# Kernel tuning notes

Measured on AMD Instinct MI355X. Metric: run time of the kernel, lower is better.

The kernel has to match this reference:

```python
import jax, jax.numpy as jnp
import numpy as np

B, T, E, H, C = 64, 256, 1024, 1024, 32000


def setup_inputs() -> dict:
    key = jax.random.key(0)
    ks = jax.random.split(key, 8)
    s = 0.02
    return {
        "X": jax.random.randint(ks[0], (B, T), 0, C),
        "emb": jax.random.normal(ks[1], (C, E), jnp.float32) * s,
        "Wi1": jax.random.normal(ks[2], (4, H, E), jnp.float32) * s,
        "Wh1": jax.random.normal(ks[3], (4, H, H), jnp.float32) * s,
        "bi1": jnp.ones((4, H), jnp.float32),
        "bh1": jnp.ones((4, H), jnp.float32),
        "Wi2": jax.random.normal(ks[4], (4, H, E), jnp.float32) * s,
        "Wh2": jax.random.normal(ks[5], (4, H, H), jnp.float32) * s,
        "bi2": jnp.ones((4, H), jnp.float32),
        "bh2": jnp.ones((4, H), jnp.float32),
        "W": jax.random.normal(ks[6], (C, H), jnp.float32) * s,
        "b": jnp.ones((C,), jnp.float32),
    }


def _lstm_last_o(x_tbe, Wi, Wh, bi, bh):
    """Run LSTM over time; return the LAST output gate o_T, shape [B, H].

    x_tbe: [T, B, E]; Wi: [4, H, E]; Wh: [4, H, H]; bi, bh: [4, H]
    Gate order g = 0:i, 1:f, 2:g(cell cand), 3:o. Original module adds BOTH
    biases (b_i_* + b_h_*) every step.
    """
    Tn, Bn = x_tbe.shape[0], x_tbe.shape[1]
    Hn = Wh.shape[1]
    # Precompute input projections for all timesteps: [T, B, 4, H]
    xp = jnp.einsum('tbe,ghe->tbgh', x_tbe, Wi) + bi + bh

    def step(carry, xp_t):
        h, c, _ = carry
        g = xp_t + jnp.einsum('bh,gkh->bgk', h, Wh)  # [B, 4, H]
        i_t = jax.nn.sigmoid(g[:, 0])
        f_t = jax.nn.sigmoid(g[:, 1])
        g_t = jnp.tanh(g[:, 2])
        o_t = jax.nn.sigmoid(g[:, 3])
        c_new = f_t * c + i_t * g_t
        h_new = o_t * jnp.tanh(c_new)
        return (h_new, c_new, o_t), None

    z = jnp.zeros((Bn, Hn), x_tbe.dtype)
    (h_f, c_f, o_f), _ = jax.lax.scan(step, (z, z, z), xp)
    return o_f


def reference(X, emb, Wi1, Wh1, bi1, bh1, Wi2, Wh2, bi2, bh2, W, b):
    x = emb[X]                     # [B, T, E]
    xt = jnp.transpose(x, (1, 0, 2))  # [T, B, E]
    o1 = _lstm_last_o(xt, Wi1, Wh1, bi1, bh1)           # forward direction
    o2 = _lstm_last_o(xt[::-1], Wi2, Wh2, bi2, bh2)     # reversed direction
    return (o1 + o2) @ W.T + b      # [B, n_class]
```

## Files before the change

### kernel.cpp

```cpp
#include <hip/hip_runtime.h>
#include <hip/hip_bf16.h>
#include <stdint.h>

typedef __attribute__((ext_vector_type(4))) float    f32x4;
typedef __attribute__((ext_vector_type(8))) short    bf16x8;
typedef __attribute__((ext_vector_type(4))) uint32_t u32x4;
typedef unsigned short u16;

#define T_   256
#define B_   64
#define E_   1024
#define H_   1024
#define CLS  32000
#define NWG  256

#define OFF_XBF   0ull
#define OFF_CNT   OFF_XBF
#define OFF_WIALL 33554432ull
#define OFF_XP    50331648ull
#define OFF_WHP   318767104ull
#define OFF_BSUM  335544320ull
#define OFF_OBUF  336101376ull
#define OFF_OSUM  336625664ull
#define OFF_HROT  336756736ull
#define HROT_END  404127744ull

__device__ __forceinline__ u16 f2bf(float f) {
    union { float f; uint32_t i; } v; v.f = f;
    uint32_t r = v.i + 0x7fffu + ((v.i >> 16) & 1u);
    return (u16)(r >> 16);
}
__device__ __forceinline__ float bf2f(u16 u) {
    union { uint32_t i; float f; } v; v.i = ((uint32_t)u) << 16; return v.f;
}
__device__ __forceinline__ float sigm(float x)   { return 1.f / (1.f + __expf(-x)); }
__device__ __forceinline__ float tanh_f(float x) { return 1.f - 2.f / (__expf(2.f * x) + 1.f); }

__device__ __forceinline__ void ldg4_cc(unsigned& d, const unsigned* p) {
    asm volatile("global_load_dword %0, %1, off sc0 sc1"
                 : "=v"(d) : "v"(p) : "memory");
}
__device__ __forceinline__ void stg16_cc(u16* p, bf16x8 v) {
    asm volatile("global_store_dwordx4 %0, %1, off sc0 sc1"
                 :: "v"(p), "v"(v) : "memory");
}
__device__ __forceinline__ void stg4_cc(unsigned* p, unsigned v) {
    asm volatile("global_store_dword %0, %1, off sc0 sc1"
                 :: "v"(p), "v"(v) : "memory");
}
__device__ __forceinline__ void wait_vm0() {
    asm volatile("s_waitcnt vmcnt(0)" ::: "memory");
}


__global__ void k_gather(const int* __restrict__ X, const float* __restrict__ emb,
                         u16* __restrict__ xbf) {
    const int m = blockIdx.x;
    const int t = m >> 6, b = m & 63;
    const int tok = X[b * T_ + t];
    const float* src = emb + (size_t)tok * E_;
    u16* dst = xbf + (size_t)m * E_;
    const int e = threadIdx.x * 4;
    float4 v = *(const float4*)(src + e);
    ushort4 o; o.x = f2bf(v.x); o.y = f2bf(v.y); o.z = f2bf(v.z); o.w = f2bf(v.w);
    *(ushort4*)(dst + e) = o;
}

__global__ void k_cvt(const float* __restrict__ src, u16* __restrict__ dst) {
    const int i = (blockIdx.x * 256 + threadIdx.x) * 4;
    float4 v = *(const float4*)(src + i);
    ushort4 o; o.x = f2bf(v.x); o.y = f2bf(v.y); o.z = f2bf(v.z); o.w = f2bf(v.w);
    *(ushort4*)(dst + i) = o;
}

__global__ void k_packwh(const float* __restrict__ Wh1, const float* __restrict__ Wh2,
                         u16* __restrict__ whp) {
    const int gi  = blockIdx.x * 256 + threadIdx.x;
    const int wg  = gi >> 12;
    const int lin = gi & 4095;
    const int kc  = lin & 127;
    const int col = lin >> 7;
    const int dir = wg >> 7, hblk = wg & 127;
    const int g = col >> 3, hh = col & 7;
    const float* src = (dir ? Wh2 : Wh1) + (size_t)(g * H_ + hblk * 8 + hh) * H_ + kc * 8;
    float4 v0 = *(const float4*)(src);
    float4 v1 = *(const float4*)(src + 4);
    const uint32_t boff = (uint32_t)(((kc * 32 + col) * 16) ^ ((kc & 3) << 4));
    u16* dst = whp + (size_t)wg * 32768 + boff / 2;
    ushort4 o0, o1;
    o0.x = f2bf(v0.x); o0.y = f2bf(v0.y); o0.z = f2bf(v0.z); o0.w = f2bf(v0.w);
    o1.x = f2bf(v1.x); o1.y = f2bf(v1.y); o1.z = f2bf(v1.z); o1.w = f2bf(v1.w);
    *(ushort4*)dst = o0;
    *(ushort4*)(dst + 4) = o1;
}

__global__ void k_bias(const float* __restrict__ bi1, const float* __restrict__ bh1,
                       const float* __restrict__ bi2, const float* __restrict__ bh2,
                       float* __restrict__ bsum) {
    const int i = blockIdx.x * 256 + threadIdx.x;
    bsum[i] = (i < 4096) ? (bi1[i] + bh1[i]) : (bi2[i - 4096] + bh2[i - 4096]);
}


#define GLDS16(gp, lp) __builtin_amdgcn_global_load_lds( \
    (const __attribute__((address_space(1))) uint32_t*)(gp), \
    (__attribute__((address_space(3))) uint32_t*)(lp), 16, 0, 0)

__global__ __launch_bounds__(256) void k_gemm_xp(const u16* __restrict__ A,
                                                 const u16* __restrict__ Bw,
                                                 u16* __restrict__ Cp) {
    __shared__ __align__(16) u16 As[128 * 32];
    __shared__ __align__(16) u16 Bs[128 * 32];
    const int bid = blockIdx.x;
    const int bn = bid & 63, bm = bid >> 6;
    const int tid = threadIdx.x;
    const int wid = tid >> 6, lane = tid & 63;
    const int wm = wid & 1, wn = wid >> 1;
    const int col16 = lane & 15, kslot = lane >> 4;
    const char* Abase = (const char*)A + (size_t)bm * 128 * 2048;
    const char* Bbase = (const char*)Bw + (size_t)bn * 128 * 2048;
    const int rowoff = (lane >> 2) * 2048 + (lane & 3) * 16;
    f32x4 acc[4][4] = {};
    for (int kt = 0; kt < 32; ++kt) {
        const int ko = kt * 64;
#pragma unroll
        for (int q = 0; q < 2; ++q) {
            const int ci = q * 4 + wid;
            GLDS16(Abase + (size_t)ci * 16 * 2048 + rowoff + ko, (char*)As + ci * 1024);
            GLDS16(Bbase + (size_t)ci * 16 * 2048 + rowoff + ko, (char*)Bs + ci * 1024);
        }
        __syncthreads();
        bf16x8 af[4], bfr[4];
#pragma unroll
        for (int mi = 0; mi < 4; ++mi)
            af[mi] = *(const bf16x8*)(As + (wm * 64 + mi * 16 + col16) * 32 + kslot * 8);
#pragma unroll
        for (int ni = 0; ni < 4; ++ni)
            bfr[ni] = *(const bf16x8*)(Bs + (wn * 64 + ni * 16 + col16) * 32 + kslot * 8);
#pragma unroll
        for (int mi = 0; mi < 4; ++mi)
#pragma unroll
            for (int ni = 0; ni < 4; ++ni)
                acc[mi][ni] = __builtin_amdgcn_mfma_f32_16x16x32_bf16(af[mi], bfr[ni], acc[mi][ni], 0, 0, 0);
        __syncthreads();
    }
#pragma unroll
    for (int mi = 0; mi < 4; ++mi)
#pragma unroll
        for (int ni = 0; ni < 4; ++ni)
#pragma unroll
            for (int q = 0; q < 4; ++q) {
                const int r  = bm * 128 + wm * 64 + mi * 16 + kslot * 4 + q;
                const int cn = bn * 128 + wn * 64 + ni * 16 + col16;
                const int dircol = cn >> 12, c = cn & 4095;
                const int g = c >> 10, hidx = c & 1023;
                const int wgc = dircol * 128 + (hidx >> 3), fhc = hidx & 7;
                Cp[((size_t)r * 256 + wgc) * 32 + fhc * 4 + g] = f2bf(acc[mi][ni][q]);
            }
}

__global__ __launch_bounds__(512, 1) void k_lstm(
    const u16* __restrict__ xp, const u16* __restrict__ whp,
    const float* __restrict__ bsum, u16* hrot,
    float* __restrict__ obuf, unsigned* cnt) {
    __shared__ __align__(16) u16 wlds[32768];
    __shared__ float glds[2][64][35];
    __shared__ __align__(16) u16 hxch[64][8];
    const int wg = blockIdx.x;
    const int dir = wg >> 7, hblk = wg & 127;
    const int tid = threadIdx.x;
    const int wid = tid >> 6, lane = tid & 63;
    const int mtile = wid & 3, khalf = wid >> 2;
    const int col16 = lane & 15, kslot = lane >> 4;
    {
        const u32x4* s = (const u32x4*)(whp + (size_t)wg * 32768);
        u32x4* d = (u32x4*)wlds;
#pragma unroll
        for (int i = 0; i < 8; ++i) d[tid + i * 512] = s[tid + i * 512];
    }
    const int fb = tid >> 3, fh = tid & 7;
    const int hidx = hblk * 8 + fh;
    const int arow = mtile * 16 + col16;
    float bsF[4];
#pragma unroll
    for (int g = 0; g < 4; ++g) bsF[g] = bsum[dir * 4096 + g * 1024 + hidx];
    const unsigned* pollp = cnt + (size_t)(dir * 128 + khalf * 64 + lane) * 32;
    unsigned* flag_own = cnt + (size_t)(dir * 128 + hblk) * 32;
    float cc = 0.f;
    ushort4 xv;
    xv = *(const ushort4*)(xp + ((size_t)((dir ? (T_ - 1) : 0) * 64 + fb) * 256 + wg) * 32 + fh * 4);
    __syncthreads();
    for (int s = 0; s < T_; ++s) {
        if (s > 0) {
            const unsigned target = (unsigned)s;
            for (;;) {
                unsigned f;
                ldg4_cc(f, pollp);
                wait_vm0();
                if (__all(f >= target)) break;
                __builtin_amdgcn_s_sleep(1);
            }
        }
        __builtin_amdgcn_sched_barrier(0);
        const u16* hbase = hrot + (size_t)(s * 2 + dir) * 131072
                         + (size_t)(khalf * 64) * 512 + arow * 8;
        bf16x8 hf[16];
#pragma unroll
        for (int kk = 0; kk < 16; ++kk)
            hf[kk] = *(const bf16x8*)(hbase + (size_t)(kk * 4 + kslot) * 512);
        f32x4 acc0 = {0.f, 0.f, 0.f, 0.f}, acc1 = {0.f, 0.f, 0.f, 0.f};
#pragma unroll
        for (int kk = 0; kk < 16; ++kk) {
            const int kc = khalf * 64 + kk * 4 + kslot;
            const uint32_t base = (uint32_t)(kc * 512);
            const uint32_t sw = (uint32_t)((kc & 3) << 4);
            bf16x8 b0 = *(const bf16x8*)((const char*)wlds + ((base + (uint32_t)(col16 * 16)) ^ sw));
            bf16x8 b1 = *(const bf16x8*)((const char*)wlds + ((base + (uint32_t)(256 + col16 * 16)) ^ sw));
            acc0 = __builtin_amdgcn_mfma_f32_16x16x32_bf16(hf[kk], b0, acc0, 0, 0, 0);
            acc1 = __builtin_amdgcn_mfma_f32_16x16x32_bf16(hf[kk], b1, acc1, 0, 0, 0);
        }
#pragma unroll
        for (int q = 0; q < 4; ++q) {
            glds[khalf][mtile * 16 + kslot * 4 + q][col16]      = acc0[q];
            glds[khalf][mtile * 16 + kslot * 4 + q][16 + col16] = acc1[q];
        }
        __syncthreads();
        const float gi = glds[0][fb][fh]      + glds[1][fb][fh]      + bsF[0] + bf2f(xv.x);
        const float gf = glds[0][fb][8 + fh]  + glds[1][fb][8 + fh]  + bsF[1] + bf2f(xv.y);
        const float gc = glds[0][fb][16 + fh] + glds[1][fb][16 + fh] + bsF[2] + bf2f(xv.z);
        const float go = glds[0][fb][24 + fh] + glds[1][fb][24 + fh] + bsF[3] + bf2f(xv.w);
        const float iv = sigm(gi), fv = sigm(gf), gv = tanh_f(gc), ov = sigm(go);
        cc = fv * cc + iv * gv;
        const float hv = ov * tanh_f(cc);
        hxch[fb][fh] = f2bf(hv);
        if (s == T_ - 1) obuf[(size_t)(dir * 64 + fb) * 1024 + hidx] = ov;
        __syncthreads();
        if (wid == 0) {
            bf16x8 hv8 = *(const bf16x8*)(&hxch[lane][0]);
            u16* hst = hrot + (size_t)((s + 1) * 2 + dir) * 131072
                     + (size_t)hblk * 512 + lane * 8;
            stg16_cc(hst, hv8);
            wait_vm0();
            if (lane == 0) stg4_cc(flag_own, (unsigned)(s + 1));
        }
        if (s < T_ - 1) {
            const int tn = dir ? (T_ - 2 - s) : (s + 1);
            xv = *(const ushort4*)(xp + ((size_t)(tn * 64 + fb) * 256 + wg) * 32 + fh * 4);
        }
    }
}


__global__ void k_osum(const float* __restrict__ obuf, u16* __restrict__ osum) {
    const int i = blockIdx.x * 256 + threadIdx.x;
    osum[i] = f2bf(obuf[i] + obuf[65536 + i]);
}

__global__ __launch_bounds__(256) void k_cls(const u16* __restrict__ osum,
                                             const float* __restrict__ W,
                                             const float* __restrict__ bias,
                                             float* __restrict__ out) {
    const int blk = blockIdx.x;
    const int tid = threadIdx.x, wid = tid >> 6, lane = tid & 63;
    const int col16 = lane & 15, kslot = lane >> 4;
    const int ncol0 = blk * 128 + wid * 32;
    f32x4 acc[4][2] = {};
    for (int kk = 0; kk < 32; ++kk) {
        const int kof = kk * 32 + kslot * 8;
        bf16x8 a[4];
#pragma unroll
        for (int mi = 0; mi < 4; ++mi)
            a[mi] = *(const bf16x8*)(osum + (mi * 16 + col16) * 1024 + kof);
#pragma unroll
        for (int nt = 0; nt < 2; ++nt) {
            const float* wr = W + (size_t)(ncol0 + nt * 16 + col16) * 1024 + kof;
            float4 w0 = *(const float4*)wr;
            float4 w1 = *(const float4*)(wr + 4);
            union { bf16x8 v; u16 u[8]; } bb;
            bb.u[0] = f2bf(w0.x); bb.u[1] = f2bf(w0.y); bb.u[2] = f2bf(w0.z); bb.u[3] = f2bf(w0.w);
            bb.u[4] = f2bf(w1.x); bb.u[5] = f2bf(w1.y); bb.u[6] = f2bf(w1.z); bb.u[7] = f2bf(w1.w);
#pragma unroll
            for (int mi = 0; mi < 4; ++mi)
                acc[mi][nt] = __builtin_amdgcn_mfma_f32_16x16x32_bf16(a[mi], bb.v, acc[mi][nt], 0, 0, 0);
        }
    }
#pragma unroll
    for (int nt = 0; nt < 2; ++nt) {
        const int cn = ncol0 + nt * 16 + col16;
        const float bv = bias[cn];
#pragma unroll
        for (int mi = 0; mi < 4; ++mi)
#pragma unroll
            for (int q = 0; q < 4; ++q)
                out[(size_t)(mi * 16 + kslot * 4 + q) * CLS + cn] = acc[mi][nt][q] + bv;
    }
}


extern "C" void kernel_launch(void* const* d_in, const int* in_sizes, int n_in,
                              void* d_out, int out_size, void* d_ws, size_t ws_size,
                              hipStream_t stream) {
    const int*   X   = (const int*)d_in[0];
    const float* emb = (const float*)d_in[1];
    const float* Wi1 = (const float*)d_in[2];
    const float* Wh1 = (const float*)d_in[3];
    const float* bi1 = (const float*)d_in[4];
    const float* bh1 = (const float*)d_in[5];
    const float* Wi2 = (const float*)d_in[6];
    const float* Wh2 = (const float*)d_in[7];
    const float* bi2 = (const float*)d_in[8];
    const float* bh2 = (const float*)d_in[9];
    const float* W   = (const float*)d_in[10];
    const float* bb  = (const float*)d_in[11];
    float* out = (float*)d_out;
    char* ws = (char*)d_ws;

    u16*      xbf   = (u16*)(ws + OFF_XBF);
    u16*      wiall = (u16*)(ws + OFF_WIALL);
    u16*      xpb   = (u16*)(ws + OFF_XP);
    u16*      whp   = (u16*)(ws + OFF_WHP);
    float*    bsum  = (float*)(ws + OFF_BSUM);
    float*    obuf  = (float*)(ws + OFF_OBUF);
    u16*      osum  = (u16*)(ws + OFF_OSUM);
    u16*      hrot  = (u16*)(ws + OFF_HROT);
    unsigned* cnt   = (unsigned*)(ws + OFF_CNT);

    k_gather<<<dim3(16384), dim3(256), 0, stream>>>(X, emb, xbf);
    k_cvt<<<dim3(4096), dim3(256), 0, stream>>>(Wi1, wiall);
    k_cvt<<<dim3(4096), dim3(256), 0, stream>>>(Wi2, wiall + 4194304);
    k_packwh<<<dim3(4096), dim3(256), 0, stream>>>(Wh1, Wh2, whp);
    k_bias<<<dim3(32), dim3(256), 0, stream>>>(bi1, bh1, bi2, bh2, bsum);
    hipMemsetAsync(hrot, 0, 262144, stream);
    k_gemm_xp<<<dim3(8192), dim3(256), 0, stream>>>(xbf, wiall, xpb);
    hipMemsetAsync(cnt, 0, 32768, stream);
    {
        const u16* xp_p = xpb; const u16* whp_p = whp; const float* bs_p = bsum;
        u16* hr_p = hrot; float* ob_p = obuf; unsigned* cnt_p = cnt;
        void* args[] = { (void*)&xp_p, (void*)&whp_p, (void*)&bs_p,
                         (void*)&hr_p, (void*)&ob_p, (void*)&cnt_p };
        hipError_t e = hipLaunchCooperativeKernel((void*)k_lstm, dim3(NWG), dim3(512),
                                                  args, 0, stream);
        if (e != hipSuccess) {
            k_lstm<<<dim3(NWG), dim3(512), 0, stream>>>(xpb, whp, bsum, hrot, obuf, cnt);
        }
    }
    k_osum<<<dim3(256), dim3(256), 0, stream>>>(obuf, osum);
    k_cls<<<dim3(250), dim3(256), 0, stream>>>(osum, W, bb, out);
    (void)in_sizes; (void)n_in; (void)out_size; (void)ws_size;
}
```

Before: 1.782 ms.

## Use per-wave subflags and XCD-aware block mapping in LSTM recurrence sync

Each wave now writes its h values directly to global memory with short stores and publishes its own per-wave subflag. This removes the LDS exchange and one workgroup barrier per step. Pollers read 8 subflags per producer with vector loads, and only one wave per k-half polls global memory while the others spin on an LDS release word. Workgroups are remapped so each direction's blocks share XCDs, and the next-step xp load is issued earlier to overlap with the poll. The risks are more flag traffic and finer-grained stores, plus correctness that depends on memory-ordering assumptions between waves.

```diff
diff --git a/kernel.cpp b/kernel.cpp
--- a/kernel.cpp
+++ b/kernel.cpp
@@ -36,13 +36,13 @@
 __device__ __forceinline__ float sigm(float x)   { return 1.f / (1.f + __expf(-x)); }
 __device__ __forceinline__ float tanh_f(float x) { return 1.f - 2.f / (__expf(2.f * x) + 1.f); }
 
-__device__ __forceinline__ void ldg4_cc(unsigned& d, const unsigned* p) {
-    asm volatile("global_load_dword %0, %1, off sc0 sc1"
+__device__ __forceinline__ void ldg16u_cc(u32x4& d, const unsigned* p) {
+    asm volatile("global_load_dwordx4 %0, %1, off sc0 sc1"
                  : "=v"(d) : "v"(p) : "memory");
 }
-__device__ __forceinline__ void stg16_cc(u16* p, bf16x8 v) {
-    asm volatile("global_store_dwordx4 %0, %1, off sc0 sc1"
-                 :: "v"(p), "v"(v) : "memory");
+__device__ __forceinline__ void stg2_cc(u16* p, u16 v) {
+    asm volatile("global_store_short %0, %1, off sc0 sc1"
+                 :: "v"(p), "v"((uint32_t)v) : "memory");
 }
 __device__ __forceinline__ void stg4_cc(unsigned* p, unsigned v) {
     asm volatile("global_store_dword %0, %1, off sc0 sc1"
@@ -165,15 +165,18 @@
     float* __restrict__ obuf, unsigned* cnt) {
     __shared__ __align__(16) u16 wlds[32768];
     __shared__ float glds[2][64][35];
-    __shared__ __align__(16) u16 hxch[64][8];
-    const int wg = blockIdx.x;
-    const int dir = wg >> 7, hblk = wg & 127;
+    __shared__ int lds_rel[2];
+    const int pwg = blockIdx.x;
+    const int xcd = pwg & 7;
+    const int dir = xcd >> 2;
+    const int hblk = (pwg >> 3) * 4 + (xcd & 3);
+    const int lwg = dir * 128 + hblk;
     const int tid = threadIdx.x;
     const int wid = tid >> 6, lane = tid & 63;
     const int mtile = wid & 3, khalf = wid >> 2;
     const int col16 = lane & 15, kslot = lane >> 4;
     {
-        const u32x4* s = (const u32x4*)(whp + (size_t)wg * 32768);
+        const u32x4* s = (const u32x4*)(whp + (size_t)lwg * 32768);
         u32x4* d = (u32x4*)wlds;
 #pragma unroll
         for (int i = 0; i < 8; ++i) d[tid + i * 512] = s[tid + i * 512];
@@ -184,30 +187,48 @@
     float bsF[4];
 #pragma unroll
     for (int g = 0; g < 4; ++g) bsF[g] = bsum[dir * 4096 + g * 1024 + hidx];
-    const unsigned* pollp = cnt + (size_t)(dir * 128 + khalf * 64 + lane) * 32;
-    unsigned* flag_own = cnt + (size_t)(dir * 128 + hblk) * 32;
+    const unsigned* pollp = cnt + dir * 1024 + khalf * 512 + lane * 8;
+    unsigned* subflag = cnt + dir * 1024 + hblk * 8 + wid;
+    if (tid < 2) lds_rel[tid] = 0;
     float cc = 0.f;
-    ushort4 xv;
-    xv = *(const ushort4*)(xp + ((size_t)((dir ? (T_ - 1) : 0) * 64 + fb) * 256 + wg) * 32 + fh * 4);
+    ushort4 xv, xvn;
+    xv = *(const ushort4*)(xp + ((size_t)((dir ? (T_ - 1) : 0) * 64 + fb) * 256 + lwg) * 32 + fh * 4);
     __syncthreads();
     for (int s = 0; s < T_; ++s) {
         if (s > 0) {
-            const unsigned target = (unsigned)s;
-            for (;;) {
-                unsigned f;
-                ldg4_cc(f, pollp);
-                wait_vm0();
-                if (__all(f >= target)) break;
-                __builtin_amdgcn_s_sleep(1);
+            if (mtile == 0) {
+                const unsigned t = (unsigned)s;
+                for (;;) {
+                    u32x4 f0, f1;
+                    ldg16u_cc(f0, pollp);
+                    ldg16u_cc(f1, pollp + 4);
+                    wait_vm0();
+                    const bool ok = f0[0] >= t && f0[1] >= t && f0[2] >= t && f0[3] >= t &&
+                                    f1[0] >= t && f1[1] >= t && f1[2] >= t && f1[3] >= t;
+                    if (__all(ok)) break;
+                    __builtin_amdgcn_s_sleep(1);
+                }
+                if (lane == 0)
+                    __hip_atomic_store(&lds_rel[khalf], s, __ATOMIC_RELAXED,
+                                       __HIP_MEMORY_SCOPE_WORKGROUP);
+            } else {
+                while (__hip_atomic_load(&lds_rel[khalf], __ATOMIC_RELAXED,
+                                         __HIP_MEMORY_SCOPE_WORKGROUP) < s)
+                    __builtin_amdgcn_s_sleep(1);
             }
-        }
-        __builtin_amdgcn_sched_barrier(0);
-        const u16* hbase = hrot + (size_t)(s * 2 + dir) * 131072
-                         + (size_t)(khalf * 64) * 512 + arow * 8;
+            __builtin_amdgcn_sched_barrier(0);
+        }
+        if (s < T_ - 1) {
+            const int tn = dir ? (T_ - 2 - s) : (s + 1);
+            xvn = *(const ushort4*)(xp + ((size_t)(tn * 64 + fb) * 256 + lwg) * 32 + fh * 4);
+        }
+        const u16* hbase = hrot + (size_t)(s * 2 + dir) * 131072;
         bf16x8 hf[16];
 #pragma unroll
-        for (int kk = 0; kk < 16; ++kk)
-            hf[kk] = *(const bf16x8*)(hbase + (size_t)(kk * 4 + kslot) * 512);
+        for (int kk = 0; kk < 16; ++kk) {
+            const int kc = khalf * 64 + kk * 4 + kslot;
+            hf[kk] = *(const bf16x8*)(hbase + (size_t)kc * 512 + arow * 8);
+        }
         f32x4 acc0 = {0.f, 0.f, 0.f, 0.f}, acc1 = {0.f, 0.f, 0.f, 0.f};
 #pragma unroll
         for (int kk = 0; kk < 16; ++kk) {
@@ -232,21 +253,11 @@
         const float iv = sigm(gi), fv = sigm(gf), gv = tanh_f(gc), ov = sigm(go);
         cc = fv * cc + iv * gv;
         const float hv = ov * tanh_f(cc);
-        hxch[fb][fh] = f2bf(hv);
+        stg2_cc(hrot + (size_t)((s + 1) * 2 + dir) * 131072 + hblk * 512 + tid, f2bf(hv));
         if (s == T_ - 1) obuf[(size_t)(dir * 64 + fb) * 1024 + hidx] = ov;
-        __syncthreads();
-        if (wid == 0) {
-            bf16x8 hv8 = *(const bf16x8*)(&hxch[lane][0]);
-            u16* hst = hrot + (size_t)((s + 1) * 2 + dir) * 131072
-                     + (size_t)hblk * 512 + lane * 8;
-            stg16_cc(hst, hv8);
-            wait_vm0();
-            if (lane == 0) stg4_cc(flag_own, (unsigned)(s + 1));
-        }
-        if (s < T_ - 1) {
-            const int tn = dir ? (T_ - 2 - s) : (s + 1);
-            xv = *(const ushort4*)(xp + ((size_t)(tn * 64 + fb) * 256 + wg) * 32 + fh * 4);
-        }
+        wait_vm0();
+        if (lane == 0) stg4_cc(subflag, (unsigned)(s + 1));
+        xv = xvn;
     }
 }
 
@@ -332,7 +343,7 @@
     k_bias<<<dim3(32), dim3(256), 0, stream>>>(bi1, bh1, bi2, bh2, bsum);
     hipMemsetAsync(hrot, 0, 262144, stream);
     k_gemm_xp<<<dim3(8192), dim3(256), 0, stream>>>(xbf, wiall, xpb);
-    hipMemsetAsync(cnt, 0, 32768, stream);
+    hipMemsetAsync(cnt, 0, 8192, stream);
     {
         const u16* xp_p = xpb; const u16* whp_p = whp; const float* bs_p = bsum;
         u16* hr_p = hrot; float* ob_p = obuf; unsigned* cnt_p = cnt;
```

Measured after the change: 2.231 ms. 25.2% more time.

## Fuse input projection GEMM into recurrent LSTM kernel with both weights in LDS

Applied to the files above, without the earlier changes.

Removes the separate input-projection GEMM and its large bf16 xp intermediate. Each LSTM workgroup now keeps both its Wi and Wh slices in LDS (128 KB) and does the x·Wi MFMAs inside every timestep, loading the embedded tokens for that step directly. This cuts a big GEMM launch and the write and read-back of the xp buffer. In exchange, each serial recurrent step doubles its MFMA and LDS work and issues extra global loads on the latency-critical path.

```diff
diff --git a/kernel.cpp b/kernel.cpp
--- a/kernel.cpp
+++ b/kernel.cpp
@@ -15,23 +15,17 @@
 #define NWG  256
 
 #define OFF_XBF   0ull
-#define OFF_CNT   OFF_XBF
-#define OFF_WIALL 33554432ull
-#define OFF_XP    50331648ull
-#define OFF_WHP   318767104ull
-#define OFF_BSUM  335544320ull
-#define OFF_OBUF  336101376ull
-#define OFF_OSUM  336625664ull
-#define OFF_HROT  336756736ull
-#define HROT_END  404127744ull
+#define OFF_WHP   33554432ull
+#define OFF_FLG   67108864ull
+#define OFF_BSUM  67141632ull
+#define OFF_OBUF  67174400ull
+#define OFF_OSUM  67698688ull
+#define OFF_HROT  67829760ull
 
 __device__ __forceinline__ u16 f2bf(float f) {
     union { float f; uint32_t i; } v; v.f = f;
     uint32_t r = v.i + 0x7fffu + ((v.i >> 16) & 1u);
     return (u16)(r >> 16);
-}
-__device__ __forceinline__ float bf2f(u16 u) {
-    union { uint32_t i; float f; } v; v.i = ((uint32_t)u) << 16; return v.f;
 }
 __device__ __forceinline__ float sigm(float x)   { return 1.f / (1.f + __expf(-x)); }
 __device__ __forceinline__ float tanh_f(float x) { return 1.f - 2.f / (__expf(2.f * x) + 1.f); }
@@ -66,27 +60,24 @@
     *(ushort4*)(dst + e) = o;
 }
 
-__global__ void k_cvt(const float* __restrict__ src, u16* __restrict__ dst) {
-    const int i = (blockIdx.x * 256 + threadIdx.x) * 4;
-    float4 v = *(const float4*)(src + i);
-    ushort4 o; o.x = f2bf(v.x); o.y = f2bf(v.y); o.z = f2bf(v.z); o.w = f2bf(v.w);
-    *(ushort4*)(dst + i) = o;
-}
-
-__global__ void k_packwh(const float* __restrict__ Wh1, const float* __restrict__ Wh2,
-                         u16* __restrict__ whp) {
+__global__ void k_packw(const float* __restrict__ Wi1, const float* __restrict__ Wh1,
+                        const float* __restrict__ Wi2, const float* __restrict__ Wh2,
+                        u16* __restrict__ whp) {
     const int gi  = blockIdx.x * 256 + threadIdx.x;
-    const int wg  = gi >> 12;
-    const int lin = gi & 4095;
+    const int half = gi >> 20;
+    const int r   = gi & 1048575;
+    const int wg  = r >> 12;
+    const int lin = r & 4095;
     const int kc  = lin & 127;
     const int col = lin >> 7;
     const int dir = wg >> 7, hblk = wg & 127;
     const int g = col >> 3, hh = col & 7;
-    const float* src = (dir ? Wh2 : Wh1) + (size_t)(g * H_ + hblk * 8 + hh) * H_ + kc * 8;
+    const float* W = half ? (dir ? Wh2 : Wh1) : (dir ? Wi2 : Wi1);
+    const float* src = W + (size_t)(g * H_ + hblk * 8 + hh) * H_ + kc * 8;
     float4 v0 = *(const float4*)(src);
     float4 v1 = *(const float4*)(src + 4);
     const uint32_t boff = (uint32_t)(((kc * 32 + col) * 16) ^ ((kc & 3) << 4));
-    u16* dst = whp + (size_t)wg * 32768 + boff / 2;
+    u16* dst = whp + (size_t)wg * 65536 + half * 32768 + boff / 2;
     ushort4 o0, o1;
     o0.x = f2bf(v0.x); o0.y = f2bf(v0.y); o0.z = f2bf(v0.z); o0.w = f2bf(v0.w);
     o1.x = f2bf(v1.x); o1.y = f2bf(v1.y); o1.z = f2bf(v1.z); o1.w = f2bf(v1.w);
@@ -101,69 +92,11 @@
     bsum[i] = (i < 4096) ? (bi1[i] + bh1[i]) : (bi2[i - 4096] + bh2[i - 4096]);
 }
 
-
-#define GLDS16(gp, lp) __builtin_amdgcn_global_load_lds( \
-    (const __attribute__((address_space(1))) uint32_t*)(gp), \
-    (__attribute__((address_space(3))) uint32_t*)(lp), 16, 0, 0)
-
-__global__ __launch_bounds__(256) void k_gemm_xp(const u16* __restrict__ A,
-                                                 const u16* __restrict__ Bw,
-                                                 u16* __restrict__ Cp) {
-    __shared__ __align__(16) u16 As[128 * 32];
-    __shared__ __align__(16) u16 Bs[128 * 32];
-    const int bid = blockIdx.x;
-    const int bn = bid & 63, bm = bid >> 6;
-    const int tid = threadIdx.x;
-    const int wid = tid >> 6, lane = tid & 63;
-    const int wm = wid & 1, wn = wid >> 1;
-    const int col16 = lane & 15, kslot = lane >> 4;
-    const char* Abase = (const char*)A + (size_t)bm * 128 * 2048;
-    const char* Bbase = (const char*)Bw + (size_t)bn * 128 * 2048;
-    const int rowoff = (lane >> 2) * 2048 + (lane & 3) * 16;
-    f32x4 acc[4][4] = {};
-    for (int kt = 0; kt < 32; ++kt) {
-        const int ko = kt * 64;
-#pragma unroll
-        for (int q = 0; q < 2; ++q) {
-            const int ci = q * 4 + wid;
-            GLDS16(Abase + (size_t)ci * 16 * 2048 + rowoff + ko, (char*)As + ci * 1024);
-            GLDS16(Bbase + (size_t)ci * 16 * 2048 + rowoff + ko, (char*)Bs + ci * 1024);
-        }
-        __syncthreads();
-        bf16x8 af[4], bfr[4];
-#pragma unroll
-        for (int mi = 0; mi < 4; ++mi)
-            af[mi] = *(const bf16x8*)(As + (wm * 64 + mi * 16 + col16) * 32 + kslot * 8);
-#pragma unroll
-        for (int ni = 0; ni < 4; ++ni)
-            bfr[ni] = *(const bf16x8*)(Bs + (wn * 64 + ni * 16 + col16) * 32 + kslot * 8);
-#pragma unroll
-        for (int mi = 0; mi < 4; ++mi)
-#pragma unroll
-            for (int ni = 0; ni < 4; ++ni)
-                acc[mi][ni] = __builtin_amdgcn_mfma_f32_16x16x32_bf16(af[mi], bfr[ni], acc[mi][ni], 0, 0, 0);
-        __syncthreads();
-    }
-#pragma unroll
-    for (int mi = 0; mi < 4; ++mi)
-#pragma unroll
-        for (int ni = 0; ni < 4; ++ni)
-#pragma unroll
-            for (int q = 0; q < 4; ++q) {
-                const int r  = bm * 128 + wm * 64 + mi * 16 + kslot * 4 + q;
-                const int cn = bn * 128 + wn * 64 + ni * 16 + col16;
-                const int dircol = cn >> 12, c = cn & 4095;
-                const int g = c >> 10, hidx = c & 1023;
-                const int wgc = dircol * 128 + (hidx >> 3), fhc = hidx & 7;
-                Cp[((size_t)r * 256 + wgc) * 32 + fhc * 4 + g] = f2bf(acc[mi][ni][q]);
-            }
-}
-
 __global__ __launch_bounds__(512, 1) void k_lstm(
-    const u16* __restrict__ xp, const u16* __restrict__ whp,
+    const u16* __restrict__ xbf, const u16* __restrict__ whp,
     const float* __restrict__ bsum, u16* hrot,
     float* __restrict__ obuf, unsigned* cnt) {
-    __shared__ __align__(16) u16 wlds[32768];
+    __shared__ __align__(16) u16 wlds[65536];
     __shared__ float glds[2][64][35];
     __shared__ __align__(16) u16 hxch[64][8];
     const int wg = blockIdx.x;
@@ -173,10 +106,10 @@
     const int mtile = wid & 3, khalf = wid >> 2;
     const int col16 = lane & 15, kslot = lane >> 4;
     {
-        const u32x4* s = (const u32x4*)(whp + (size_t)wg * 32768);
+        const u32x4* s = (const u32x4*)(whp + (size_t)wg * 65536);
         u32x4* d = (u32x4*)wlds;
 #pragma unroll
-        for (int i = 0; i < 8; ++i) d[tid + i * 512] = s[tid + i * 512];
+        for (int i = 0; i < 16; ++i) d[tid + i * 512] = s[tid + i * 512];
     }
     const int fb = tid >> 3, fh = tid & 7;
     const int hidx = hblk * 8 + fh;
@@ -187,10 +120,14 @@
     const unsigned* pollp = cnt + (size_t)(dir * 128 + khalf * 64 + lane) * 32;
     unsigned* flag_own = cnt + (size_t)(dir * 128 + hblk) * 32;
     float cc = 0.f;
-    ushort4 xv;
-    xv = *(const ushort4*)(xp + ((size_t)((dir ? (T_ - 1) : 0) * 64 + fb) * 256 + wg) * 32 + fh * 4);
     __syncthreads();
     for (int s = 0; s < T_; ++s) {
+        const int t = dir ? (T_ - 1 - s) : s;
+        const u16* xrow = xbf + (size_t)(t * 64 + arow) * 1024 + khalf * 512;
+        bf16x8 xa[16];
+#pragma unroll
+        for (int kk = 0; kk < 16; ++kk)
+            xa[kk] = *(const bf16x8*)(xrow + kk * 32 + kslot * 8);
         if (s > 0) {
             const unsigned target = (unsigned)s;
             for (;;) {
@@ -216,6 +153,16 @@
             const uint32_t sw = (uint32_t)((kc & 3) << 4);
             bf16x8 b0 = *(const bf16x8*)((const char*)wlds + ((base + (uint32_t)(col16 * 16)) ^ sw));
             bf16x8 b1 = *(const bf16x8*)((const char*)wlds + ((base + (uint32_t)(256 + col16 * 16)) ^ sw));
+            acc0 = __builtin_amdgcn_mfma_f32_16x16x32_bf16(xa[kk], b0, acc0, 0, 0, 0);
+            acc1 = __builtin_amdgcn_mfma_f32_16x16x32_bf16(xa[kk], b1, acc1, 0, 0, 0);
+        }
+#pragma unroll
+        for (int kk = 0; kk < 16; ++kk) {
+            const int kc = khalf * 64 + kk * 4 + kslot;
+            const uint32_t base = (uint32_t)(65536 + kc * 512);
+            const uint32_t sw = (uint32_t)((kc & 3) << 4);
+            bf16x8 b0 = *(const bf16x8*)((const char*)wlds + ((base + (uint32_t)(col16 * 16)) ^ sw));
+            bf16x8 b1 = *(const bf16x8*)((const char*)wlds + ((base + (uint32_t)(256 + col16 * 16)) ^ sw));
             acc0 = __builtin_amdgcn_mfma_f32_16x16x32_bf16(hf[kk], b0, acc0, 0, 0, 0);
             acc1 = __builtin_amdgcn_mfma_f32_16x16x32_bf16(hf[kk], b1, acc1, 0, 0, 0);
         }
@@ -225,10 +172,10 @@
             glds[khalf][mtile * 16 + kslot * 4 + q][16 + col16] = acc1[q];
         }
         __syncthreads();
-        const float gi = glds[0][fb][fh]      + glds[1][fb][fh]      + bsF[0] + bf2f(xv.x);
-        const float gf = glds[0][fb][8 + fh]  + glds[1][fb][8 + fh]  + bsF[1] + bf2f(xv.y);
-        const float gc = glds[0][fb][16 + fh] + glds[1][fb][16 + fh] + bsF[2] + bf2f(xv.z);
-        const float go = glds[0][fb][24 + fh] + glds[1][fb][24 + fh] + bsF[3] + bf2f(xv.w);
+        const float gi = glds[0][fb][fh]      + glds[1][fb][fh]      + bsF[0];
+        const float gf = glds[0][fb][8 + fh]  + glds[1][fb][8 + fh]  + bsF[1];
+        const float gc = glds[0][fb][16 + fh] + glds[1][fb][16 + fh] + bsF[2];
+        const float go = glds[0][fb][24 + fh] + glds[1][fb][24 + fh] + bsF[3];
         const float iv = sigm(gi), fv = sigm(gf), gv = tanh_f(gc), ov = sigm(go);
         cc = fv * cc + iv * gv;
         const float hv = ov * tanh_f(cc);
@@ -242,10 +189,6 @@
             stg16_cc(hst, hv8);
             wait_vm0();
             if (lane == 0) stg4_cc(flag_own, (unsigned)(s + 1));
-        }
-        if (s < T_ - 1) {
-            const int tn = dir ? (T_ - 2 - s) : (s + 1);
-            xv = *(const ushort4*)(xp + ((size_t)(tn * 64 + fb) * 256 + wg) * 32 + fh * 4);
         }
     }
 }
@@ -316,32 +259,27 @@
     char* ws = (char*)d_ws;
 
     u16*      xbf   = (u16*)(ws + OFF_XBF);
-    u16*      wiall = (u16*)(ws + OFF_WIALL);
-    u16*      xpb   = (u16*)(ws + OFF_XP);
     u16*      whp   = (u16*)(ws + OFF_WHP);
+    unsigned* cnt   = (unsigned*)(ws + OFF_FLG);
     float*    bsum  = (float*)(ws + OFF_BSUM);
     float*    obuf  = (float*)(ws + OFF_OBUF);
     u16*      osum  = (u16*)(ws + OFF_OSUM);
     u16*      hrot  = (u16*)(ws + OFF_HROT);
-    unsigned* cnt   = (unsigned*)(ws + OFF_CNT);
 
     k_gather<<<dim3(16384), dim3(256), 0, stream>>>(X, emb, xbf);
-    k_cvt<<<dim3(4096), dim3(256), 0, stream>>>(Wi1, wiall);
-    k_cvt<<<dim3(4096), dim3(256), 0, stream>>>(Wi2, wiall + 4194304);
-    k_packwh<<<dim3(4096), dim3(256), 0, stream>>>(Wh1, Wh2, whp);
+    k_packw<<<dim3(8192), dim3(256), 0, stream>>>(Wi1, Wh1, Wi2, Wh2, whp);
     k_bias<<<dim3(32), dim3(256), 0, stream>>>(bi1, bh1, bi2, bh2, bsum);
     hipMemsetAsync(hrot, 0, 262144, stream);
-    k_gemm_xp<<<dim3(8192), dim3(256), 0, stream>>>(xbf, wiall, xpb);
     hipMemsetAsync(cnt, 0, 32768, stream);
     {
-        const u16* xp_p = xpb; const u16* whp_p = whp; const float* bs_p = bsum;
+        const u16* xb_p = xbf; const u16* whp_p = whp; const float* bs_p = bsum;
         u16* hr_p = hrot; float* ob_p = obuf; unsigned* cnt_p = cnt;
-        void* args[] = { (void*)&xp_p, (void*)&whp_p, (void*)&bs_p,
+        void* args[] = { (void*)&xb_p, (void*)&whp_p, (void*)&bs_p,
                          (void*)&hr_p, (void*)&ob_p, (void*)&cnt_p };
         hipError_t e = hipLaunchCooperativeKernel((void*)k_lstm, dim3(NWG), dim3(512),
                                                   args, 0, stream);
         if (e != hipSuccess) {
-            k_lstm<<<dim3(NWG), dim3(512), 0, stream>>>(xpb, whp, bsum, hrot, obuf, cnt);
+            k_lstm<<<dim3(NWG), dim3(512), 0, stream>>>(xbf, whp, bsum, hrot, obuf, cnt);
         }
     }
     k_osum<<<dim3(256), dim3(256), 0, stream>>>(obuf, osum);
```

Measured after the change: 1.753 ms. Within noise of the previous version (-1.7%).
